# Kernel tuning notes

Hardware: AMD Instinct MI355X
Metric: run time of the kernel (lower is better)

The kernel has to match this reference:

```python
import jax, jax.numpy as jnp
import numpy as np

H0, H1, NHID, BATCH = 256, 256, 512, 2048

def setup_inputs() -> dict:
    key = jax.random.key(0)
    k1, k2, k3, k4, k5 = jax.random.split(key, 5)
    initrange = 0.1
    inputs = jax.random.normal(k1, (BATCH, NHID), dtype=jnp.float32)
    labels = jax.random.randint(k2, (BATCH,), 0, H1, dtype=jnp.int32)
    parent_labels = jax.random.randint(k3, (BATCH,), 0, H0, dtype=jnp.int32)
    layer_top_W = jax.random.uniform(k4, (NHID, H0), jnp.float32, -initrange, initrange)
    layer_top_b = jnp.zeros((H0,), jnp.float32)
    layer_bottom_W = jax.random.uniform(k5, (H0, NHID, H1), jnp.float32, -initrange, initrange)
    layer_bottom_b = jnp.zeros((H0, H1), jnp.float32)
    return {"inputs": inputs, "labels": labels, "parent_labels": parent_labels,
            "layer_top_W": layer_top_W, "layer_top_b": layer_top_b,
            "layer_bottom_W": layer_bottom_W, "layer_bottom_b": layer_bottom_b}

def reference(inputs, labels, parent_labels, layer_top_W, layer_top_b,
              layer_bottom_W, layer_bottom_b):
    batch = inputs.shape[0]
    # top-level softmax over coarse classes: [B, H0]
    top_probs = jax.nn.softmax(inputs @ layer_top_W + layer_top_b, axis=1)
    # per-sample gather of expert weight slice [B, NHID, H1] then bmm
    Wb = layer_bottom_W[parent_labels]            # [B, NHID, H1]
    bb = layer_bottom_b[parent_labels]            # [B, H1]
    bottom_logits = jnp.einsum('bd,bdk->bk', inputs, Wb) + bb
    bottom_probs = jax.nn.softmax(bottom_logits, axis=1)
    ar = jnp.arange(batch)
    target_probs = top_probs[ar, parent_labels] * bottom_probs[ar, labels]
    return target_probs
```

## Files before the change

kernel.cpp:

```cpp
#include <hip/hip_runtime.h>

constexpr int BATCH = 2048;
constexpr int NHID  = 512;
constexpr int H0    = 256;
constexpr int H1    = 256;
constexpr int KCH   = 4;
constexpr int DCH   = NHID / KCH;
constexpr int S     = 16;
constexpr int LSTRIDE = 2048;
constexpr int NBOT  = H0 * KCH;
constexpr int NTOP  = (BATCH / S) * KCH;


__global__ __launch_bounds__(256) void k_prep(const int* __restrict__ parents,
                                              int* __restrict__ list,
                                              int* __restrict__ nval) {
    const int p = blockIdx.x, t = threadIdx.x, g = t >> 6, l = t & 63;
    __shared__ int wcnt[4];
    int running = 0;
    for (int c = 0; c < BATCH; c += 256) {
        const bool match = (parents[c + t] == p);
        const unsigned long long mask = __ballot(match);
        if (l == 0) wcnt[g] = __popcll(mask);
        __syncthreads();
        int off = running;
        for (int w = 0; w < g; ++w) off += wcnt[w];
        if (match)
            list[p * LSTRIDE + off + __popcll(mask & ((1ull << l) - 1ull))] = c + t;
        running += wcnt[0] + wcnt[1] + wcnt[2] + wcnt[3];
        __syncthreads();
    }
    if (t == 0) nval[p] = running;
}

__device__ __forceinline__ void gemv_tile(const float* __restrict__ Wp,
                                          const float xs[S][DCH],
                                          float4 acc[S]) {
    float4 ring[8];
    #pragma unroll
    for (int i = 0; i < 8; ++i)
        ring[i] = *(const float4*)(Wp + (size_t)i * 256);

    for (int d = 0; d < DCH; d += 8) {
        #pragma unroll
        for (int h = 0; h < 2; ++h) {
            const int dd = d + 4 * h;
            const float4 w0 = ring[4 * h + 0], w1 = ring[4 * h + 1];
            const float4 w2 = ring[4 * h + 2], w3 = ring[4 * h + 3];
            if (dd + 8 < DCH) {
                #pragma unroll
                for (int i = 0; i < 4; ++i)
                    ring[4 * h + i] =
                        *(const float4*)(Wp + (size_t)(dd + 8 + i) * 256);
            }
            #pragma unroll
            for (int s = 0; s < S; ++s) {
                const float4 xv = *(const float4*)&xs[s][dd];
                float4 a = acc[s];
                a.x = fmaf(xv.x, w0.x, a.x); a.y = fmaf(xv.x, w0.y, a.y);
                a.z = fmaf(xv.x, w0.z, a.z); a.w = fmaf(xv.x, w0.w, a.w);
                a.x = fmaf(xv.y, w1.x, a.x); a.y = fmaf(xv.y, w1.y, a.y);
                a.z = fmaf(xv.y, w1.z, a.z); a.w = fmaf(xv.y, w1.w, a.w);
                a.x = fmaf(xv.z, w2.x, a.x); a.y = fmaf(xv.z, w2.y, a.y);
                a.z = fmaf(xv.z, w2.z, a.z); a.w = fmaf(xv.z, w2.w, a.w);
                a.x = fmaf(xv.w, w3.x, a.x); a.y = fmaf(xv.w, w3.y, a.y);
                a.z = fmaf(xv.w, w3.z, a.z); a.w = fmaf(xv.w, w3.w, a.w);
                acc[s] = a;
            }
        }
    }
}

__global__ __launch_bounds__(64) void k_gemv(
    const float* __restrict__ x, const float* __restrict__ topW,
    const float* __restrict__ botW, const int* __restrict__ list,
    const int* __restrict__ nval, float* __restrict__ wstop,
    float* __restrict__ wsbot) {
    const int b = blockIdx.x, l = threadIdx.x;
    __shared__ __align__(16) float xs[S][DCH];
    __shared__ int sid[S];

    if (b < NBOT) {
        const int p = b >> 2, k = b & 3;
        const int n = nval[p];
        const float* W = botW + ((size_t)p * NHID + (size_t)k * DCH) * H1 + 4 * l;
        for (int tb = 0; tb < n; tb += S) {
            const int rem = min(S, n - tb);
            for (int i = l; i < S; i += 64)
                sid[i] = list[p * LSTRIDE + tb + min(i, rem - 1)];
            __syncthreads();
            for (int i = l; i < S * (DCH / 4); i += 64) {
                const int s = i >> 5, c = i & 31;
                ((float4*)xs[s])[c] =
                    *(const float4*)(x + (size_t)sid[s] * NHID + k * DCH + 4 * c);
            }
            __syncthreads();
            float4 acc[S];
            #pragma unroll
            for (int s = 0; s < S; ++s) acc[s] = make_float4(0.f, 0.f, 0.f, 0.f);
            gemv_tile(W, xs, acc);
            for (int s = 0; s < rem; ++s)
                *(float4*)(wsbot + ((size_t)sid[s] * KCH + k) * H1 + 4 * l) = acc[s];
            __syncthreads();
        }
    } else {
        const int bb = b - NBOT, j = bb >> 2, k = bb & 3;
        const float* W = topW + (size_t)k * DCH * H0 + 4 * l;
        for (int i = l; i < S * (DCH / 4); i += 64) {
            const int s = i >> 5, c = i & 31;
            ((float4*)xs[s])[c] =
                *(const float4*)(x + (size_t)(S * j + s) * NHID + k * DCH + 4 * c);
        }
        __syncthreads();
        float4 acc[S];
        #pragma unroll
        for (int s = 0; s < S; ++s) acc[s] = make_float4(0.f, 0.f, 0.f, 0.f);
        gemv_tile(W, xs, acc);
        #pragma unroll
        for (int s = 0; s < S; ++s)
            *(float4*)(wstop + ((size_t)(S * j + s) * KCH + k) * H0 + 4 * l) = acc[s];
    }
}

__global__ __launch_bounds__(64) void k_fin(
    const int* __restrict__ labels, const int* __restrict__ parents,
    const float* __restrict__ topb, const float* __restrict__ botb,
    const float* __restrict__ wstop, const float* __restrict__ wsbot,
    float* __restrict__ out) {
    const int s = blockIdx.x, l = threadIdx.x;
    const int par = parents[s];
    float pr[2];
    #pragma unroll
    for (int pass = 0; pass < 2; ++pass) {
        const float* wsrc = pass ? wsbot : wstop;
        float4 v = make_float4(0.f, 0.f, 0.f, 0.f);
        #pragma unroll
        for (int k = 0; k < KCH; ++k) {
            const float4 c = *(const float4*)(wsrc + ((size_t)s * KCH + k) * 256 + 4 * l);
            v.x += c.x; v.y += c.y; v.z += c.z; v.w += c.w;
        }
        const float4 bias = pass ? *(const float4*)(botb + (size_t)par * H1 + 4 * l)
                                 : *(const float4*)(topb + 4 * l);
        v.x += bias.x; v.y += bias.y; v.z += bias.z; v.w += bias.w;

        float m = fmaxf(fmaxf(v.x, v.y), fmaxf(v.z, v.w));
        #pragma unroll
        for (int off = 32; off > 0; off >>= 1)
            m = fmaxf(m, __shfl_xor(m, off, 64));

        const float ex = expf(v.x - m), ey = expf(v.y - m);
        const float ez = expf(v.z - m), ew = expf(v.w - m);
        float sum = (ex + ey) + (ez + ew);
        #pragma unroll
        for (int off = 32; off > 0; off >>= 1)
            sum += __shfl_xor(sum, off, 64);

        const int tgt = pass ? labels[s] : par;
        const int c0 = 4 * l;
        float et = (c0 == tgt) ? ex : (c0 + 1 == tgt) ? ey
                 : (c0 + 2 == tgt) ? ez : (c0 + 3 == tgt) ? ew : 0.f;
        #pragma unroll
        for (int off = 32; off > 0; off >>= 1)
            et += __shfl_xor(et, off, 64);

        pr[pass] = et / sum;
    }
    if (l == 0) out[s] = pr[0] * pr[1];
}

extern "C" void kernel_launch(void* const* d_in, const int* in_sizes, int n_in,
                              void* d_out, int out_size, void* d_ws, size_t ws_size,
                              hipStream_t stream) {
    const float* x       = (const float*)d_in[0];
    const int*   labels  = (const int*)  d_in[1];
    const int*   parents = (const int*)  d_in[2];
    const float* topW    = (const float*)d_in[3];
    const float* topb    = (const float*)d_in[4];
    const float* botW    = (const float*)d_in[5];
    const float* botb    = (const float*)d_in[6];
    float*       out     = (float*)d_out;

    int*   list  = (int*)d_ws;
    int*   nval  = (int*)((char*)d_ws + (size_t)H0 * LSTRIDE * sizeof(int));
    float* wstop = (float*)((char*)d_ws + (size_t)H0 * LSTRIDE * sizeof(int) + 4096);
    float* wsbot = wstop + (size_t)BATCH * KCH * H0;

    k_prep<<<H0, 256, 0, stream>>>(parents, list, nval);
    k_gemv<<<NBOT + NTOP, 64, 0, stream>>>(x, topW, botW, list, nval, wstop, wsbot);
    k_fin<<<BATCH, 64, 0, stream>>>(labels, parents, topb, botb, wstop, wsbot, out);
}
```

Baseline: 245.0 us.

## Pack four independent wave work units per block and split reduction dimension finer

The hidden dimension is now split into 8 chunks instead of 4, and the sample tile is halved to 8. Each 256-thread block now runs four independent single-wave work units, which lets the block-wide barriers be dropped in favour of wave-local staging. The inner GEMV loads 8 weight rows per step instead of using a rolling prefetch ring. This raises parallelism and occupancy on the weight-streaming pass, but it doubles the partial-sum workspace and traffic. Parents with more than 8 samples now read their weights more than once, and the wave-local shared-memory use relies on lockstep execution without explicit barriers.

```diff
diff --git a/kernel.cpp b/kernel.cpp
--- a/kernel.cpp
+++ b/kernel.cpp
@@ -4,12 +4,10 @@
 constexpr int NHID  = 512;
 constexpr int H0    = 256;
 constexpr int H1    = 256;
-constexpr int KCH   = 4;
+constexpr int KCH   = 8;
 constexpr int DCH   = NHID / KCH;
-constexpr int S     = 16;
+constexpr int S     = 8;
 constexpr int LSTRIDE = 2048;
-constexpr int NBOT  = H0 * KCH;
-constexpr int NTOP  = (BATCH / S) * KCH;
 
 
 __global__ __launch_bounds__(256) void k_prep(const int* __restrict__ parents,
@@ -33,101 +31,87 @@
     if (t == 0) nval[p] = running;
 }
 
-__device__ __forceinline__ void gemv_tile(const float* __restrict__ Wp,
-                                          const float xs[S][DCH],
-                                          float4 acc[S]) {
-    float4 ring[8];
-    #pragma unroll
-    for (int i = 0; i < 8; ++i)
-        ring[i] = *(const float4*)(Wp + (size_t)i * 256);
-
+__device__ __forceinline__ void chunk_gemv(const float* __restrict__ W,
+                                           const float* __restrict__ xw,
+                                           int l, float4 acc[S]) {
     for (int d = 0; d < DCH; d += 8) {
+        float4 wt[8];
         #pragma unroll
-        for (int h = 0; h < 2; ++h) {
-            const int dd = d + 4 * h;
-            const float4 w0 = ring[4 * h + 0], w1 = ring[4 * h + 1];
-            const float4 w2 = ring[4 * h + 2], w3 = ring[4 * h + 3];
-            if (dd + 8 < DCH) {
-                #pragma unroll
-                for (int i = 0; i < 4; ++i)
-                    ring[4 * h + i] =
-                        *(const float4*)(Wp + (size_t)(dd + 8 + i) * 256);
-            }
+        for (int r = 0; r < 8; ++r)
+            wt[r] = *(const float4*)(W + (size_t)(d + r) * 256 + 4 * l);
+        #pragma unroll
+        for (int r = 0; r < 8; ++r) {
             #pragma unroll
             for (int s = 0; s < S; ++s) {
-                const float4 xv = *(const float4*)&xs[s][dd];
-                float4 a = acc[s];
-                a.x = fmaf(xv.x, w0.x, a.x); a.y = fmaf(xv.x, w0.y, a.y);
-                a.z = fmaf(xv.x, w0.z, a.z); a.w = fmaf(xv.x, w0.w, a.w);
-                a.x = fmaf(xv.y, w1.x, a.x); a.y = fmaf(xv.y, w1.y, a.y);
-                a.z = fmaf(xv.y, w1.z, a.z); a.w = fmaf(xv.y, w1.w, a.w);
-                a.x = fmaf(xv.z, w2.x, a.x); a.y = fmaf(xv.z, w2.y, a.y);
-                a.z = fmaf(xv.z, w2.z, a.z); a.w = fmaf(xv.z, w2.w, a.w);
-                a.x = fmaf(xv.w, w3.x, a.x); a.y = fmaf(xv.w, w3.y, a.y);
-                a.z = fmaf(xv.w, w3.z, a.z); a.w = fmaf(xv.w, w3.w, a.w);
-                acc[s] = a;
+                const float xv = xw[s * DCH + d + r];
+                acc[s].x = fmaf(xv, wt[r].x, acc[s].x);
+                acc[s].y = fmaf(xv, wt[r].y, acc[s].y);
+                acc[s].z = fmaf(xv, wt[r].z, acc[s].z);
+                acc[s].w = fmaf(xv, wt[r].w, acc[s].w);
             }
         }
     }
 }
 
-__global__ __launch_bounds__(64) void k_gemv(
+__global__ __launch_bounds__(256) void k_gemv(
     const float* __restrict__ x, const float* __restrict__ topW,
     const float* __restrict__ botW, const int* __restrict__ list,
     const int* __restrict__ nval, float* __restrict__ wstop,
     float* __restrict__ wsbot) {
-    const int b = blockIdx.x, l = threadIdx.x;
-    __shared__ __align__(16) float xs[S][DCH];
-    __shared__ int sid[S];
+    const int w = threadIdx.x >> 6, l = threadIdx.x & 63;
+    const int u = blockIdx.x * 4 + w;
+    __shared__ __align__(16) float xs[4][S][DCH];
+    __shared__ int sid[4][S];
+    float* xw = &xs[w][0][0];
 
-    if (b < NBOT) {
-        const int p = b >> 2, k = b & 3;
+    if (u < H0 * KCH) {
+        const int p = u >> 3, k = u & 7;
         const int n = nval[p];
-        const float* W = botW + ((size_t)p * NHID + (size_t)k * DCH) * H1 + 4 * l;
+        const float* W = botW + ((size_t)p * NHID + (size_t)k * DCH) * H1;
         for (int tb = 0; tb < n; tb += S) {
             const int rem = min(S, n - tb);
-            for (int i = l; i < S; i += 64)
-                sid[i] = list[p * LSTRIDE + tb + min(i, rem - 1)];
-            __syncthreads();
-            for (int i = l; i < S * (DCH / 4); i += 64) {
-                const int s = i >> 5, c = i & 31;
-                ((float4*)xs[s])[c] =
-                    *(const float4*)(x + (size_t)sid[s] * NHID + k * DCH + 4 * c);
+            if (l < S) sid[w][l] = list[p * LSTRIDE + tb + min(l, rem - 1)];
+            #pragma unroll
+            for (int i0 = 0; i0 < 2; ++i0) {
+                const int i = i0 * 64 + l, s = i >> 4, c = i & 15;
+                const int row = list[p * LSTRIDE + tb + min(s, rem - 1)];
+                *(float4*)&xs[w][s][4 * c] =
+                    *(const float4*)(x + (size_t)row * NHID + k * DCH + 4 * c);
             }
-            __syncthreads();
             float4 acc[S];
             #pragma unroll
             for (int s = 0; s < S; ++s) acc[s] = make_float4(0.f, 0.f, 0.f, 0.f);
-            gemv_tile(W, xs, acc);
+            chunk_gemv(W, xw, l, acc);
             for (int s = 0; s < rem; ++s)
-                *(float4*)(wsbot + ((size_t)sid[s] * KCH + k) * H1 + 4 * l) = acc[s];
-            __syncthreads();
+                *(float4*)(wsbot + ((size_t)sid[w][s] * KCH + k) * H1 + 4 * l) = acc[s];
         }
     } else {
-        const int bb = b - NBOT, j = bb >> 2, k = bb & 3;
-        const float* W = topW + (size_t)k * DCH * H0 + 4 * l;
-        for (int i = l; i < S * (DCH / 4); i += 64) {
-            const int s = i >> 5, c = i & 31;
-            ((float4*)xs[s])[c] =
+        const int u2 = u - H0 * KCH;
+        const int j = u2 >> 3, k = u2 & 7;
+        const float* W = topW + (size_t)k * DCH * H0;
+        #pragma unroll
+        for (int i0 = 0; i0 < 2; ++i0) {
+            const int i = i0 * 64 + l, s = i >> 4, c = i & 15;
+            *(float4*)&xs[w][s][4 * c] =
                 *(const float4*)(x + (size_t)(S * j + s) * NHID + k * DCH + 4 * c);
         }
-        __syncthreads();
         float4 acc[S];
         #pragma unroll
         for (int s = 0; s < S; ++s) acc[s] = make_float4(0.f, 0.f, 0.f, 0.f);
-        gemv_tile(W, xs, acc);
+        chunk_gemv(W, xw, l, acc);
         #pragma unroll
         for (int s = 0; s < S; ++s)
             *(float4*)(wstop + ((size_t)(S * j + s) * KCH + k) * H0 + 4 * l) = acc[s];
     }
 }
 
-__global__ __launch_bounds__(64) void k_fin(
+__global__ __launch_bounds__(256) void k_fin(
     const int* __restrict__ labels, const int* __restrict__ parents,
     const float* __restrict__ topb, const float* __restrict__ botb,
     const float* __restrict__ wstop, const float* __restrict__ wsbot,
     float* __restrict__ out) {
-    const int s = blockIdx.x, l = threadIdx.x;
+    const int w = threadIdx.x >> 6, l = threadIdx.x & 63;
+    const int s = blockIdx.x * 4 + w;
     const int par = parents[s];
     float pr[2];
     #pragma unroll
@@ -186,6 +170,7 @@
     float* wsbot = wstop + (size_t)BATCH * KCH * H0;
 
     k_prep<<<H0, 256, 0, stream>>>(parents, list, nval);
-    k_gemv<<<NBOT + NTOP, 64, 0, stream>>>(x, topW, botW, list, nval, wstop, wsbot);
-    k_fin<<<BATCH, 64, 0, stream>>>(labels, parents, topb, botb, wstop, wsbot, out);
+    const int units = H0 * KCH + (BATCH / S) * KCH;
+    k_gemv<<<units / 4, 256, 0, stream>>>(x, topW, botW, list, nval, wstop, wsbot);
+    k_fin<<<BATCH / 4, 256, 0, stream>>>(labels, parents, topb, botb, wstop, wsbot, out);
 }
```

Result: no change. 249.7 us (+1.9%).
